# Kernel optimization log

Hardware: AMD Instinct MI355X
Metric: run time of the kernel (lower is better)

## Reference

```python
import jax, jax.numpy as jnp
import numpy as np

PAD = 2
EPS = 1e-5


def setup_inputs() -> dict:
    key = jax.random.key(0)
    k1, = jax.random.split(key, 1)
    N, C, H, W = 32, 64, 224, 224
    x = jax.random.normal(k1, (N, C, H, W), dtype=jnp.float32)
    bn_weight = jnp.ones((C,), dtype=jnp.float32)
    bn_bias = jnp.zeros((C,), dtype=jnp.float32)
    post_scale = jnp.asarray(0.5, dtype=jnp.float32)
    return {"x": x, "bn_weight": bn_weight, "bn_bias": bn_bias, "post_scale": post_scale}


def reference(x, bn_weight, bn_bias, post_scale):
    # 1) reflection pad H and W by PAD on each side -> (N, C, H+2p, W+2p)
    pad_x = jnp.pad(x, ((0, 0), (0, 0), (PAD, PAD), (PAD, PAD)), mode="reflect")
    # 2-4) GLU over [pad_x, roll(pad_x)] along channels == pad_x * sigmoid(roll)
    pad_x_roll = jnp.roll(pad_x, shift=1, axis=1)
    gated = pad_x * jax.nn.sigmoid(pad_x_roll)
    # 5) global average pool -> (N, C)
    pooled = gated.mean(axis=(2, 3))
    # 6) BatchNorm1d (training mode: batch stats, biased variance, affine)
    mu = pooled.mean(axis=0)
    var = pooled.var(axis=0)  # biased, matches BN normalization
    normed = (pooled - mu) / jnp.sqrt(var + EPS) * bn_weight + bn_bias
    # 7-9) sigmoid reweight + channel-mean residual + scalar scale + exact GELU
    scale = jax.nn.sigmoid(normed)[:, :, None, None]
    channel_mean = pad_x.mean(axis=(2, 3), keepdims=True)
    out = jax.nn.gelu((gated * scale + channel_mean) * post_scale, approximate=False)
    return out.reshape(out.shape[0], -1)
```

## Files before the change

kernel.cpp:

```cpp
#include <hip/hip_runtime.h>
#include <math.h>

#define NB 32
#define CB 64
#define HH 224
#define WW 224
#define PADP 2
#define HP (HH + 2*PADP)
#define WP (WW + 2*PADP)
#define HW (HH*WW)
#define HWP (HP*WP)
#define EPSV 1e-5f
#define CHUNKS 49

typedef float v4f __attribute__((ext_vector_type(4)));

__device__ __forceinline__ float fsig(float v) {
    float e = __expf(-v);
    return __builtin_amdgcn_rcpf(1.0f + e);
}
__device__ __forceinline__ float fgelu(float v) {
    float t = v * (1.5957691216f + 0.0713548162f * v * v);
    return v * fsig(t);
}
__device__ __forceinline__ float edgew(int w) {
    return 1.0f + (float)((w == 1) | (w == 2) | (w == WW-3) | (w == WW-2));
}

__global__ __launch_bounds__(256) void k_pool3(const float* __restrict__ x,
                                               float* __restrict__ partG,
                                               float* __restrict__ partX) {
    int b = blockIdx.x;
    int n = b / CHUNKS;
    int chunk = b - n * CHUNKS;
    int wave = threadIdx.x >> 6;
    int lane = threadIdx.x & 63;

    int p0 = chunk * 1024 + lane * 4;
    float4 wgt[4];
    #pragma unroll
    for (int m = 0; m < 4; ++m) {
        int pm = p0 + m * 256;
        int h  = pm / WW;
        int w0 = pm - h * WW;
        float wh = 1.0f + (float)((h == 1) | (h == 2) | (h == HH-3) | (h == HH-2));
        wgt[m].x = wh * edgew(w0);
        wgt[m].y = wh * edgew(w0 + 1);
        wgt[m].z = wh * edgew(w0 + 2);
        wgt[m].w = wh * edgew(w0 + 3);
    }

    const float* xn = x + (size_t)n * CB * HW;
    int c0 = wave * 16;
    int cg = (c0 + CB - 1) & (CB - 1);
    float4 prev[4];
    #pragma unroll
    for (int m = 0; m < 4; ++m)
        prev[m] = *(const float4*)(xn + (size_t)cg * HW + p0 + m * 256);

    for (int k = 0; k < 16; ++k) {
        int c = c0 + k;
        float4 cur[4];
        #pragma unroll
        for (int m = 0; m < 4; ++m)
            cur[m] = *(const float4*)(xn + (size_t)c * HW + p0 + m * 256);
        float sG = 0.f, sX = 0.f;
        #pragma unroll
        for (int m = 0; m < 4; ++m) {
            sG += wgt[m].x * cur[m].x * fsig(prev[m].x);
            sG += wgt[m].y * cur[m].y * fsig(prev[m].y);
            sG += wgt[m].z * cur[m].z * fsig(prev[m].z);
            sG += wgt[m].w * cur[m].w * fsig(prev[m].w);
            sX += wgt[m].x * cur[m].x + wgt[m].y * cur[m].y
                + wgt[m].z * cur[m].z + wgt[m].w * cur[m].w;
            prev[m] = cur[m];
        }
        #pragma unroll
        for (int off = 32; off >= 1; off >>= 1) {
            sG += __shfl_xor(sG, off);
            sX += __shfl_xor(sX, off);
        }
        if (lane == 0) {
            size_t idx = ((size_t)n * CB + c) * CHUNKS + chunk;
            partG[idx] = sG;
            partX[idx] = sX;
        }
    }
}

__global__ __launch_bounds__(64) void k_red(const float* __restrict__ partG,
                                            const float* __restrict__ partX,
                                            float* __restrict__ pooled,
                                            float* __restrict__ cmean) {
    int bc = blockIdx.x;
    int t = threadIdx.x;
    float g = 0.f, xx = 0.f;
    if (t < CHUNKS) {
        g  = partG[(size_t)bc * CHUNKS + t];
        xx = partX[(size_t)bc * CHUNKS + t];
    }
    for (int off = 32; off >= 1; off >>= 1) {
        g  += __shfl_xor(g, off);
        xx += __shfl_xor(xx, off);
    }
    if (t == 0) {
        pooled[bc] = g  * (1.0f / (float)HWP);
        cmean[bc]  = xx * (1.0f / (float)HWP);
    }
}

__global__ __launch_bounds__(64) void k_bn(const float* __restrict__ pooled,
                                           const float* __restrict__ bnw,
                                           const float* __restrict__ bnb,
                                           float* __restrict__ scale) {
    int c = blockIdx.x;
    int t = threadIdx.x;
    float v = 0.f;
    if (t < 32) v = pooled[t * CB + c];
    float s = v;
    for (int off = 16; off >= 1; off >>= 1) s += __shfl_xor(s, off);
    float mu = s * (1.0f / 32.0f);
    float d = v - mu;
    float q = d * d;
    for (int off = 16; off >= 1; off >>= 1) q += __shfl_xor(q, off);
    float var = q * (1.0f / 32.0f);
    if (t < 32) {
        float normed = d * rsqrtf(var + EPSV) * bnw[c] + bnb[c];
        scale[t * CB + c] = 1.0f / (1.0f + expf(-normed));
    }
}

__global__ __launch_bounds__(256) void k_out(const float* __restrict__ x,
                                             const float* __restrict__ scale,
                                             const float* __restrict__ cmean,
                                             const float* __restrict__ post_scale,
                                             float* __restrict__ out) {
    int b  = blockIdx.x;
    int n  = b / HP;
    int hp = b - n * HP;
    int rh = hp - PADP; rh = rh < 0 ? -rh : (rh >= HH ? 2*HH - 2 - rh : rh);
    int wave = threadIdx.x >> 6;
    int lane = threadIdx.x & 63;
    bool act = lane < 56;
    float ps = post_scale[0];

    const float* xrow = x + (size_t)n * CB * HW + (size_t)rh * WW;
    const float* sc_row = scale + n * CB;
    const float* cm_row = cmean + n * CB;

    int c0 = wave * 16;
    int cg = (c0 + CB - 1) & (CB - 1);
    float4 prev = make_float4(0.f, 0.f, 0.f, 0.f);
    if (act) prev = *(const float4*)(xrow + (size_t)cg * HW + 4 * lane);

    for (int k = 0; k < 16; ++k) {
        int c = c0 + k;
        float4 cur = make_float4(0.f, 0.f, 0.f, 0.f);
        if (act) cur = *(const float4*)(xrow + (size_t)c * HW + 4 * lane);
        float scp = sc_row[c] * ps;
        float cmp = cm_row[c] * ps;
        float o0 = fgelu(fmaf(cur.x * fsig(prev.x), scp, cmp));
        float o1 = fgelu(fmaf(cur.y * fsig(prev.y), scp, cmp));
        float o2 = fgelu(fmaf(cur.z * fsig(prev.z), scp, cmp));
        float o3 = fgelu(fmaf(cur.w * fsig(prev.w), scp, cmp));
        float o1s = __shfl(o1, lane - 1);
        float o2s = __shfl(o2, lane - 1);
        float o3s = __shfl(o3, lane - 1);
        v4f st = { o2s, o3s, o0, o1 };
        if (lane == 0)  st = (v4f){ o2, o1, o0, o1 };
        if (lane == 56) st = (v4f){ o2s, o3s, o2s, o1s };
        if (lane < 57) {
            float* orow = out + ((size_t)n * CB + c) * HWP + (size_t)hp * WP;
            __builtin_nontemporal_store(st, (v4f*)(orow + 4 * lane));
        }
        prev = cur;
    }
}

extern "C" void kernel_launch(void* const* d_in, const int* in_sizes, int n_in,
                              void* d_out, int out_size, void* d_ws, size_t ws_size,
                              hipStream_t stream) {
    const float* x   = (const float*)d_in[0];
    const float* bnw = (const float*)d_in[1];
    const float* bnb = (const float*)d_in[2];
    const float* ps  = (const float*)d_in[3];
    float* out = (float*)d_out;

    size_t npart = (size_t)NB * CB * CHUNKS;
    float* partG  = (float*)d_ws;
    float* partX  = partG + npart;
    float* pooled = partX + npart;
    float* cmean  = pooled + NB * CB;
    float* scale  = cmean  + NB * CB;

    k_pool3<<<NB * CHUNKS, 256, 0, stream>>>(x, partG, partX);
    k_red<<<NB * CB, 64, 0, stream>>>(partG, partX, pooled, cmean);
    k_bn<<<CB, 64, 0, stream>>>(pooled, bnw, bnb, scale);
    k_out<<<NB * HP, 256, 0, stream>>>(x, scale, cmean, ps, out);
}
```

Measured before the change: 272.5 us.

## Fuse chunk reduction with batchnorm stats, remap output blocks, use nontemporal loads

The per-(n,c) chunk reduction and the batchnorm/sigmoid kernel are merged into one 64-block kernel, which drops a launch and the pooled intermediate buffer. The output kernel now permutes block indices so that consecutive blocks touch different batch images, and it reads x with nontemporal loads. The fused stats kernel runs on only 64 blocks, so it exposes little parallelism. The nontemporal loads may lose cache reuse of x rows, which are read by several blocks at the reflected padding edges.

```diff
diff --git a/kernel.cpp b/kernel.cpp
--- a/kernel.cpp
+++ b/kernel.cpp
@@ -88,43 +88,43 @@
     }
 }
 
-__global__ __launch_bounds__(64) void k_red(const float* __restrict__ partG,
-                                            const float* __restrict__ partX,
-                                            float* __restrict__ pooled,
-                                            float* __restrict__ cmean) {
-    int bc = blockIdx.x;
+__global__ __launch_bounds__(256) void k_stats(const float* __restrict__ partG,
+                                               const float* __restrict__ partX,
+                                               const float* __restrict__ bnw,
+                                               const float* __restrict__ bnb,
+                                               float* __restrict__ cmean,
+                                               float* __restrict__ scale) {
+    int c = blockIdx.x;
     int t = threadIdx.x;
+    int n = t >> 3, j0 = t & 7;
     float g = 0.f, xx = 0.f;
-    if (t < CHUNKS) {
-        g  = partG[(size_t)bc * CHUNKS + t];
-        xx = partX[(size_t)bc * CHUNKS + t];
+    for (int j = j0; j < CHUNKS; j += 8) {
+        size_t idx = ((size_t)n * CB + c) * CHUNKS + j;
+        g  += partG[idx];
+        xx += partX[idx];
     }
-    for (int off = 32; off >= 1; off >>= 1) {
+    #pragma unroll
+    for (int off = 4; off >= 1; off >>= 1) {
         g  += __shfl_xor(g, off);
         xx += __shfl_xor(xx, off);
     }
-    if (t == 0) {
-        pooled[bc] = g  * (1.0f / (float)HWP);
-        cmean[bc]  = xx * (1.0f / (float)HWP);
+    __shared__ float lG[NB];
+    if (j0 == 0) {
+        lG[n] = g;
+        cmean[n * CB + c] = xx * (1.0f / (float)HWP);
     }
-}
-
-__global__ __launch_bounds__(64) void k_bn(const float* __restrict__ pooled,
-                                           const float* __restrict__ bnw,
-                                           const float* __restrict__ bnb,
-                                           float* __restrict__ scale) {
-    int c = blockIdx.x;
-    int t = threadIdx.x;
-    float v = 0.f;
-    if (t < 32) v = pooled[t * CB + c];
-    float s = v;
-    for (int off = 16; off >= 1; off >>= 1) s += __shfl_xor(s, off);
-    float mu = s * (1.0f / 32.0f);
-    float d = v - mu;
-    float q = d * d;
-    for (int off = 16; off >= 1; off >>= 1) q += __shfl_xor(q, off);
-    float var = q * (1.0f / 32.0f);
-    if (t < 32) {
+    __syncthreads();
+    if (t < NB) {
+        float p = lG[t] * (1.0f / (float)HWP);
+        float s = p;
+        #pragma unroll
+        for (int off = 16; off >= 1; off >>= 1) s += __shfl_xor(s, off);
+        float mu = s * (1.0f / 32.0f);
+        float d = p - mu;
+        float q = d * d;
+        #pragma unroll
+        for (int off = 16; off >= 1; off >>= 1) q += __shfl_xor(q, off);
+        float var = q * (1.0f / 32.0f);
         float normed = d * rsqrtf(var + EPSV) * bnw[c] + bnb[c];
         scale[t * CB + c] = 1.0f / (1.0f + expf(-normed));
     }
@@ -135,9 +135,10 @@
                                              const float* __restrict__ cmean,
                                              const float* __restrict__ post_scale,
                                              float* __restrict__ out) {
-    int b  = blockIdx.x;
-    int n  = b / HP;
-    int hp = b - n * HP;
+    int o = blockIdx.x;
+    int w = (o & 7) * (NB * HP / 8) + (o >> 3);
+    int n  = w / HP;
+    int hp = w - n * HP;
     int rh = hp - PADP; rh = rh < 0 ? -rh : (rh >= HH ? 2*HH - 2 - rh : rh);
     int wave = threadIdx.x >> 6;
     int lane = threadIdx.x & 63;
@@ -150,13 +151,13 @@
 
     int c0 = wave * 16;
     int cg = (c0 + CB - 1) & (CB - 1);
-    float4 prev = make_float4(0.f, 0.f, 0.f, 0.f);
-    if (act) prev = *(const float4*)(xrow + (size_t)cg * HW + 4 * lane);
+    v4f prev = {0.f, 0.f, 0.f, 0.f};
+    if (act) prev = __builtin_nontemporal_load((const v4f*)(xrow + (size_t)cg * HW + 4 * lane));
 
     for (int k = 0; k < 16; ++k) {
         int c = c0 + k;
-        float4 cur = make_float4(0.f, 0.f, 0.f, 0.f);
-        if (act) cur = *(const float4*)(xrow + (size_t)c * HW + 4 * lane);
+        v4f cur = {0.f, 0.f, 0.f, 0.f};
+        if (act) cur = __builtin_nontemporal_load((const v4f*)(xrow + (size_t)c * HW + 4 * lane));
         float scp = sc_row[c] * ps;
         float cmp = cm_row[c] * ps;
         float o0 = fgelu(fmaf(cur.x * fsig(prev.x), scp, cmp));
@@ -189,12 +190,10 @@
     size_t npart = (size_t)NB * CB * CHUNKS;
     float* partG  = (float*)d_ws;
     float* partX  = partG + npart;
-    float* pooled = partX + npart;
-    float* cmean  = pooled + NB * CB;
-    float* scale  = cmean  + NB * CB;
+    float* cmean  = partX + npart;
+    float* scale  = cmean + NB * CB;
 
     k_pool3<<<NB * CHUNKS, 256, 0, stream>>>(x, partG, partX);
-    k_red<<<NB * CB, 64, 0, stream>>>(partG, partX, pooled, cmean);
-    k_bn<<<CB, 64, 0, stream>>>(pooled, bnw, bnb, scale);
+    k_stats<<<CB, 256, 0, stream>>>(partG, partX, bnw, bnb, cmean, scale);
     k_out<<<NB * HP, 256, 0, stream>>>(x, scale, cmean, ps, out);
 }
```

New measurement: 253.1 us. 1.08x faster.
